# Optimization experiments

Hardware: AMD Instinct MI355X
Metric: run time of the kernel (lower is better)

The kernel has to match this reference:

```python
import jax, jax.numpy as jnp
import numpy as np

N = 100000      # total nodes in batched graph
E_RAND = 1600000  # random edges (avg degree 16); self-loops appended -> E = E_RAND + N
B = 1024        # number of graphs / descriptor batch
DIN, D2D, D3D = 128, 200, 100
DG, DH = 20, 64
H1, H2 = 128, 32
EPS = 1e-5


def _lin_init(key, fan_in, fan_out):
    k1, k2 = jax.random.split(key)
    bound = 1.0 / np.sqrt(fan_in)
    W = jax.random.uniform(k1, (fan_in, fan_out), jnp.float32, -bound, bound)
    b = jax.random.uniform(k2, (fan_out,), jnp.float32, -bound, bound)
    return W, b


def setup_inputs() -> dict:
    key = jax.random.key(0)
    ks = jax.random.split(key, 16)
    feat = jax.random.normal(ks[0], (N, DIN), jnp.float32)
    src_r = jax.random.randint(ks[1], (E_RAND,), 0, N, jnp.int32)
    dst_r = jax.random.randint(ks[2], (E_RAND,), 0, N, jnp.int32)
    loop = jnp.arange(N, dtype=jnp.int32)
    src = jnp.concatenate([src_r, loop])  # self-loops: every node has in-degree >= 1
    dst = jnp.concatenate([dst_r, loop])
    graph_id = ((jnp.arange(N, dtype=jnp.int64) * B) // N).astype(jnp.int32)  # sorted, all B nonempty
    desc_2d = jax.random.normal(ks[3], (B, D2D), jnp.float32)
    desc_3d = jax.random.normal(ks[4], (B, D3D), jnp.float32)
    Wg1, bg1 = _lin_init(ks[5], DIN, 100)
    Wg2, bg2 = _lin_init(ks[6], 100, DG)
    Wpg, bpg = _lin_init(ks[7], DG, DH)
    Wp2, bp2 = _lin_init(ks[8], D2D, DH)
    gain = np.sqrt(6.0 / (DH + DH))
    W2 = jax.random.uniform(ks[9], (DH, DH), jnp.float32, -gain, gain)  # xavier_uniform
    Wf1, bf1 = _lin_init(ks[10], 2 * DH, H1)
    Wf2, bf2 = _lin_init(ks[11], H1, H2)
    Wf3, bf3 = _lin_init(ks[12], H2, 1)
    return dict(feat=feat, src=src, dst=dst, graph_id=graph_id,
                desc_2d=desc_2d, desc_3d=desc_3d,
                Wg1=Wg1, bg1=bg1, Wg2=Wg2, bg2=bg2,
                Wpg=Wpg, bpg=bpg, Wp2=Wp2, bp2=bp2, W2=W2,
                Wf1=Wf1, bf1=bf1, Wf2=Wf2, bf2=bf2, Wf3=Wf3, bf3=bf3,
                bn1_g=jnp.ones((H1,), jnp.float32), bn1_b=jnp.zeros((H1,), jnp.float32),
                bn2_g=jnp.ones((H2,), jnp.float32), bn2_b=jnp.zeros((H2,), jnp.float32))


def _gcn(h, W, b, src, dst):
    # copy_u -> mailbox mean: segment-mean of source feats over destination
    msg = h[src]                                               # [E, d] gather
    s = jax.ops.segment_sum(msg, dst, num_segments=N)          # [N, d]
    deg = jax.ops.segment_sum(jnp.ones((src.shape[0], 1), h.dtype), dst, num_segments=N)
    accum = s / jnp.maximum(deg, 1.0)
    return jax.nn.relu(accum @ W + b)


def _bn(x, g, b):  # BatchNorm1d, training-mode batch stats (biased var)
    mu = jnp.mean(x, axis=0)
    var = jnp.mean(jnp.square(x - mu), axis=0)
    return g * (x - mu) * jax.lax.rsqrt(var + EPS) + b


def reference(feat, src, dst, graph_id, desc_2d, desc_3d,
              Wg1, bg1, Wg2, bg2, Wpg, bpg, Wp2, bp2, W2,
              Wf1, bf1, Wf2, bf2, Wf3, bf3, bn1_g, bn1_b, bn2_g, bn2_b):
    h = _gcn(feat, Wg1, bg1, src, dst)        # relu(GCN1) -> [N,100]
    h = _gcn(h, Wg2, bg2, src, dst)           # relu(GCN2) -> [N,20]
    # dgl.mean_nodes: per-graph mean
    hs = jax.ops.segment_sum(h, graph_id, num_segments=B)
    cnt = jax.ops.segment_sum(jnp.ones((N, 1), h.dtype), graph_id, num_segments=B)
    hg = hs / jnp.maximum(cnt, 1.0)           # [B, 20]
    h_g = hg @ Wpg + bpg                      # [B, 64]
    h_d = desc_2d @ Wp2 + bp2                 # [B, 64]
    gate_vec = jax.nn.sigmoid((h_g @ W2) * h_d)
    v2 = gate_vec * h_d
    fusion = jnp.concatenate([h_g, v2], axis=-1)   # [B, 128]
    out = jax.nn.relu(_bn(fusion @ Wf1 + bf1, bn1_g, bn1_b))
    out = jax.nn.relu(_bn(out @ Wf2 + bf2, bn2_g, bn2_b))
    return out @ Wf3 + bf3                    # [B, 1]
```

## Files before the change

### kernel.cpp

```cpp
#include <hip/hip_runtime.h>
#include <math.h>

#define N_NODES 100000
#define B_GRAPH 1024
#define NBKT 391
#define NBLK 416
#define CAP 6000

typedef unsigned short ushort_t;
typedef unsigned int uint_t;
typedef __attribute__((ext_vector_type(8))) short short8v;
typedef __attribute__((ext_vector_type(4))) float f32x4;

static inline size_t alignup(size_t x){ return (x + 255) & ~(size_t)255; }

__device__ inline float bf2f(ushort_t u){
  union{ uint_t i; float f; } v; v.i = ((uint_t)u) << 16; return v.f;
}
__device__ inline float bflo(uint_t u){
  union{ uint_t i; float f; } v; v.i = u << 16; return v.f;
}
__device__ inline float bfhi(uint_t u){
  union{ uint_t i; float f; } v; v.i = u & 0xffff0000u; return v.f;
}
__device__ inline ushort_t f2bf(float f){
  union{ float f; uint_t i; } v; v.f = f;
  uint_t b = v.i;
  b += 0x7fffu + ((b >> 16) & 1u);
  return (ushort_t)(b >> 16);
}
__device__ inline uint_t packbf(float a, float b){
  return (uint_t)f2bf(a) | ((uint_t)f2bf(b) << 16);
}

__global__ __launch_bounds__(256) void k_hist(const int* __restrict__ dst,
                                              int* __restrict__ hist_g, int* __restrict__ btot,
                                              int E, int CH){
  __shared__ int h[NBKT];
  int blk = blockIdx.x, t = threadIdx.x;
  for (int i = t; i < NBKT; i += 256) h[i] = 0;
  __syncthreads();
  int s = blk*CH, e = s + CH; if (e > E) e = E;
  for (int i = s + t; i < e; i += 256) atomicAdd(&h[dst[i] >> 8], 1);
  __syncthreads();
  for (int i = t; i < NBKT; i += 256){
    int v = h[i];
    hist_g[i*NBLK + blk] = v;
    if (v) atomicAdd(&btot[i], v);
  }
}

__global__ __launch_bounds__(512) void k_scanb(const int* __restrict__ btot, int* __restrict__ bbase){
  __shared__ int sc[512];
  int t = threadIdx.x;
  int v = (t < NBKT) ? btot[t] : 0;
  sc[t] = v; __syncthreads();
  for (int off = 1; off < 512; off <<= 1){
    int u = (t >= off) ? sc[t-off] : 0;
    __syncthreads();
    sc[t] += u;
    __syncthreads();
  }
  if (t < NBKT) bbase[t] = sc[t] - v;
  if (t == NBKT-1) bbase[NBKT] = sc[t];
}

__global__ __launch_bounds__(512) void k_offs(const int* __restrict__ hist_g, const int* __restrict__ bbase,
                                              int* __restrict__ offs){
  __shared__ int sc[512];
  int b = blockIdx.x, t = threadIdx.x;
  int v = (t < NBLK) ? hist_g[b*NBLK + t] : 0;
  sc[t] = v; __syncthreads();
  for (int off = 1; off < 512; off <<= 1){
    int u = (t >= off) ? sc[t-off] : 0;
    __syncthreads();
    sc[t] += u;
    __syncthreads();
  }
  if (t < NBLK) offs[b*NBLK + t] = bbase[b] + sc[t] - v;
}

__global__ __launch_bounds__(256) void k_scatter(const int* __restrict__ src, const int* __restrict__ dst,
                                                 const int* __restrict__ offs, uint2* __restrict__ pairs,
                                                 int E, int CH){
  __shared__ int base[NBKT];
  int blk = blockIdx.x, t = threadIdx.x;
  for (int i = t; i < NBKT; i += 256) base[i] = offs[i*NBLK + blk];
  __syncthreads();
  int s = blk*CH, e = s + CH; if (e > E) e = E;
  for (int i = s + t; i < e; i += 256){
    int d = dst[i];
    int pos = atomicAdd(&base[d >> 8], 1);
    uint2 p; p.x = (uint_t)src[i]; p.y = (uint_t)d;
    pairs[pos] = p;
  }
}

__global__ __launch_bounds__(256) void k_final(const uint2* __restrict__ pairs, const int* __restrict__ bbase,
                                               int* __restrict__ rp, int* __restrict__ col){
  __shared__ uint2 buf[CAP];
  __shared__ int dcnt[256];
  __shared__ int sc[256];
  __shared__ int dpos[256];
  int b = blockIdx.x, t = threadIdx.x;
  int s = bbase[b], e = bbase[b+1], n = e - s;
  dcnt[t] = 0;
  const uint2* P;
  if (n <= CAP){
    for (int i = t; i < n; i += 256) buf[i] = pairs[s + i];
    P = buf;
  } else {
    P = pairs + s;
  }
  __syncthreads();
  for (int i = t; i < n; i += 256) atomicAdd(&dcnt[P[i].y & 255], 1);
  __syncthreads();
  int v = dcnt[t];
  sc[t] = v; __syncthreads();
  for (int off = 1; off < 256; off <<= 1){
    int u = (t >= off) ? sc[t-off] : 0;
    __syncthreads();
    sc[t] += u;
    __syncthreads();
  }
  int ex = sc[t] - v;
  int node = b*256 + t;
  if (node <= N_NODES) rp[node] = s + ex;
  dpos[t] = s + ex;
  __syncthreads();
  for (int i = t; i < n; i += 256){
    uint2 pr = P[i];
    int pos = atomicAdd(&dpos[pr.y & 255], 1);
    col[pos] = (int)pr.x;
  }
}

__global__ __launch_bounds__(256) void k_cvt(const float* __restrict__ feat, ushort_t* __restrict__ fb, int n8){
  int i = blockIdx.x*256 + threadIdx.x;
  if (i >= n8) return;
  const float4* f4 = reinterpret_cast<const float4*>(feat + (size_t)i*8);
  float4 x = f4[0], y = f4[1];
  uint4 o;
  o.x = packbf(x.x, x.y); o.y = packbf(x.z, x.w);
  o.z = packbf(y.x, y.y); o.w = packbf(y.z, y.w);
  reinterpret_cast<uint4*>(fb)[i] = o;
}

__global__ __launch_bounds__(256) void k_packw(const float* __restrict__ W, ushort_t* __restrict__ wpk){
  int idx = blockIdx.x*256 + threadIdx.x;
  if (idx >= 7*4*64) return;
  int l = idx & 63;
  int s = (idx >> 6) & 3;
  int ct = idx >> 8;
  int colj = ct*16 + (l & 15);
  int kbase = 32*s + ((l >> 4) << 3);
  #pragma unroll
  for (int j = 0; j < 8; j++){
    float w = (colj < 100) ? W[(kbase + j)*100 + colj] : 0.f;
    wpk[idx*8 + j] = f2bf(w);
  }
}

__global__ __launch_bounds__(256) void k_gemm1m(const ushort_t* __restrict__ fb, const ushort_t* __restrict__ wpk,
                                                ushort_t* __restrict__ t1, int Nn){
  int wid = threadIdx.x >> 6;
  int lane = threadIdx.x & 63;
  int rt = blockIdx.x*4 + wid;
  int row0 = rt*16;
  if (row0 >= Nn) return;
  short8v a[4];
  const ushort_t* arow = fb + (size_t)(row0 + (lane & 15))*128 + ((lane >> 4) << 3);
  #pragma unroll
  for (int s = 0; s < 4; s++)
    a[s] = *reinterpret_cast<const short8v*>(arow + 32*s);
  const short8v* bfrag = reinterpret_cast<const short8v*>(wpk);
  for (int ct = 0; ct < 7; ct++){
    f32x4 acc = {0.f, 0.f, 0.f, 0.f};
    #pragma unroll
    for (int s = 0; s < 4; s++){
      short8v b = bfrag[(ct*4 + s)*64 + lane];
      acc = __builtin_amdgcn_mfma_f32_16x16x32_bf16(a[s], b, acc, 0, 0, 0);
    }
    int colj = ct*16 + (lane & 15);
    if (colj < 100){
      ushort_t* base = t1 + colj;
      #pragma unroll
      for (int r = 0; r < 4; r++){
        int row = row0 + ((lane >> 4) << 2) + r;
        base[(size_t)row*100] = f2bf(acc[r]);
      }
    }
  }
}

__global__ __launch_bounds__(256) void k_agg1(const uint_t* __restrict__ t1u, const int* __restrict__ rp,
                                              const int* __restrict__ col, const float* __restrict__ bias,
                                              uint_t* __restrict__ h1u, int Nn){
  int lane = threadIdx.x & 63;
  int node = blockIdx.x*4 + (threadIdx.x >> 6);
  if (node >= Nn) return;
  int rs = rp[node], re = rp[node+1];
  int d2 = lane < 50 ? lane : 49;
  float slo0=0.f, slo1=0.f, shi0=0.f, shi1=0.f;
  for (int base = rs; base < re; base += 64){
    int idx = base + lane;
    int colv = col[idx < re ? idx : re-1];
    int m = re - base; if (m > 64) m = 64;
    int e = 0;
    for (; e + 4 <= m; e += 4){
      int c0 = __shfl(colv, e+0), c1 = __shfl(colv, e+1);
      int c2 = __shfl(colv, e+2), c3 = __shfl(colv, e+3);
      uint_t u0 = t1u[(size_t)c0*50 + d2];
      uint_t u1 = t1u[(size_t)c1*50 + d2];
      uint_t u2 = t1u[(size_t)c2*50 + d2];
      uint_t u3 = t1u[(size_t)c3*50 + d2];
      slo0 += bflo(u0); shi0 += bfhi(u0);
      slo1 += bflo(u1); shi1 += bfhi(u1);
      slo0 += bflo(u2); shi0 += bfhi(u2);
      slo1 += bflo(u3); shi1 += bfhi(u3);
    }
    for (; e < m; e++){
      int c = __shfl(colv, e);
      uint_t u = t1u[(size_t)c*50 + d2];
      slo0 += bflo(u); shi0 += bfhi(u);
    }
  }
  if (lane < 50){
    float inv = 1.f/(float)(re - rs);
    float vlo = (slo0 + slo1)*inv + bias[2*lane];
    float vhi = (shi0 + shi1)*inv + bias[2*lane + 1];
    vlo = vlo > 0.f ? vlo : 0.f;
    vhi = vhi > 0.f ? vhi : 0.f;
    h1u[(size_t)node*50 + lane] = packbf(vlo, vhi);
  }
}

__global__ __launch_bounds__(256) void k_gemm2(const uint_t* __restrict__ h1u, const float* __restrict__ W,
                                               ushort_t* __restrict__ t2, int Nn){
  int row = blockIdx.x*256 + threadIdx.x;
  if (row >= Nn) return;
  const uint2* xb = reinterpret_cast<const uint2*>(h1u + (size_t)row*50);
  float acc[20];
  #pragma unroll
  for (int j = 0; j < 20; j++) acc[j] = 0.f;
  #pragma unroll 5
  for (int q = 0; q < 25; q++){
    uint2 u = xb[q];
    float fx = bflo(u.x), fy = bfhi(u.x), fz = bflo(u.y), fw = bfhi(u.y);
    const float* w0 = W + q*80;
    #pragma unroll
    for (int j = 0; j < 20; j++){
      float a = acc[j];
      a = fmaf(fx, w0[j],      a);
      a = fmaf(fy, w0[20 + j], a);
      a = fmaf(fz, w0[40 + j], a);
      a = fmaf(fw, w0[60 + j], a);
      acc[j] = a;
    }
  }
  uint2* o = reinterpret_cast<uint2*>(t2 + (size_t)row*20);
  #pragma unroll
  for (int j = 0; j < 5; j++){
    uint2 v; v.x = packbf(acc[4*j], acc[4*j+1]); v.y = packbf(acc[4*j+2], acc[4*j+3]);
    o[j] = v;
  }
}

__global__ __launch_bounds__(256) void k_agg2(const uint_t* __restrict__ t2u, const int* __restrict__ rp,
                                              const int* __restrict__ col, const float* __restrict__ bias,
                                              float2* __restrict__ h2, int Nn){
  int tid = threadIdx.x;
  int node = blockIdx.x*16 + (tid >> 4);
  int l16 = tid & 15;
  if (node >= Nn) return;
  int rs = rp[node], re = rp[node+1];
  int d2 = l16 < 10 ? l16 : 9;
  int grpb = (tid & 63) & ~15;
  float slo0=0.f, slo1=0.f, shi0=0.f, shi1=0.f;
  for (int base = rs; base < re; base += 16){
    int idx = base + l16;
    int colv = col[idx < re ? idx : re-1];
    int m = re - base; if (m > 16) m = 16;
    int e = 0;
    for (; e + 4 <= m; e += 4){
      int c0 = __shfl(colv, grpb+e+0), c1 = __shfl(colv, grpb+e+1);
      int c2 = __shfl(colv, grpb+e+2), c3 = __shfl(colv, grpb+e+3);
      uint_t u0 = t2u[(size_t)c0*10 + d2];
      uint_t u1 = t2u[(size_t)c1*10 + d2];
      uint_t u2 = t2u[(size_t)c2*10 + d2];
      uint_t u3 = t2u[(size_t)c3*10 + d2];
      slo0 += bflo(u0); shi0 += bfhi(u0);
      slo1 += bflo(u1); shi1 += bfhi(u1);
      slo0 += bflo(u2); shi0 += bfhi(u2);
      slo1 += bflo(u3); shi1 += bfhi(u3);
    }
    for (; e < m; e++){
      int c = __shfl(colv, grpb+e);
      uint_t u = t2u[(size_t)c*10 + d2];
      slo0 += bflo(u); shi0 += bfhi(u);
    }
  }
  if (l16 < 10){
    float inv = 1.f/(float)(re - rs);
    float vlo = (slo0 + slo1)*inv + bias[2*l16];
    float vhi = (shi0 + shi1)*inv + bias[2*l16 + 1];
    vlo = vlo > 0.f ? vlo : 0.f;
    vhi = vhi > 0.f ? vhi : 0.f;
    float2 v; v.x = vlo; v.y = vhi;
    h2[(size_t)node*10 + l16] = v;
  }
}

__global__ __launch_bounds__(256) void k_gmean(const float* __restrict__ h2, float* __restrict__ hg){
  __shared__ float red[240];
  int g = blockIdx.x;
  int t = threadIdx.x;
  int s = (int)(((long long)g      * N_NODES + B_GRAPH - 1) / B_GRAPH);
  int e = (int)(((long long)(g+1)  * N_NODES + B_GRAPH - 1) / B_GRAPH);
  if (t < 240){
    int d  = t % 20;
    int r0 = t / 20;
    float acc = 0.f;
    for (int n = s + r0; n < e; n += 12) acc += h2[(size_t)n*20 + d];
    red[t] = acc;
  }
  __syncthreads();
  if (t < 20){
    float acc = 0.f;
    #pragma unroll
    for (int r = 0; r < 12; r++) acc += red[r*20 + t];
    hg[g*20 + t] = acc / (float)(e - s);
  }
}

__global__ __launch_bounds__(256) void k_head1(const float* __restrict__ hg, const float* __restrict__ Wpg,
                                               const float* __restrict__ bpg, const float* __restrict__ desc2,
                                               const float* __restrict__ Wp2, const float* __restrict__ bp2,
                                               float* __restrict__ hG, float* __restrict__ hD){
  int idx = blockIdx.x*256 + threadIdx.x;
  if (idx >= B_GRAPH*64) return;
  int r = idx >> 6, d = idx & 63;
  float a = bpg[d];
  for (int k = 0; k < 20; k++) a = fmaf(hg[r*20 + k], Wpg[k*64 + d], a);
  hG[r*64 + d] = a;
  float c = bp2[d];
  for (int k = 0; k < 200; k++) c = fmaf(desc2[r*200 + k], Wp2[k*64 + d], c);
  hD[r*64 + d] = c;
}

__global__ __launch_bounds__(256) void k_head2(const float* __restrict__ hG, const float* __restrict__ hD,
                                               const float* __restrict__ W2, float* __restrict__ fus){
  int idx = blockIdx.x*256 + threadIdx.x;
  if (idx >= B_GRAPH*64) return;
  int r = idx >> 6, d = idx & 63;
  float x = 0.f;
  for (int k = 0; k < 64; k++) x = fmaf(hG[r*64 + k], W2[k*64 + d], x);
  float hd = hD[r*64 + d];
  float gv = 1.f / (1.f + expf(-x*hd));
  fus[r*128 + d]      = hG[r*64 + d];
  fus[r*128 + 64 + d] = gv*hd;
}

__global__ __launch_bounds__(256) void k_tr(const float* __restrict__ X, float* __restrict__ XT){
  __shared__ float tile[32][33];
  int rb = blockIdx.x >> 2;
  int cb = blockIdx.x & 3;
  int tx = threadIdx.x & 31;
  int ty = threadIdx.x >> 5;
  #pragma unroll
  for (int i = 0; i < 4; i++){
    int r = rb*32 + ty + 8*i;
    tile[ty + 8*i][tx] = X[(size_t)r*128 + cb*32 + tx];
  }
  __syncthreads();
  #pragma unroll
  for (int i = 0; i < 4; i++){
    int c = cb*32 + ty + 8*i;
    XT[(size_t)c*1024 + rb*32 + tx] = tile[tx][ty + 8*i];
  }
}

__global__ __launch_bounds__(256) void k_bnt(const float* __restrict__ XT, const float* __restrict__ W,
                                             const float* __restrict__ bias, const float* __restrict__ gam,
                                             const float* __restrict__ bet, float* __restrict__ YT,
                                             int Kin, int Jout){
  int j = blockIdx.x;
  int t = threadIdx.x;
  float b0 = bias[j];
  float4 z; z.x = b0; z.y = b0; z.z = b0; z.w = b0;
  for (int k = 0; k < Kin; k++){
    float4 x = reinterpret_cast<const float4*>(XT + (size_t)k*1024)[t];
    float wv = W[k*Jout + j];
    z.x = fmaf(x.x, wv, z.x);
    z.y = fmaf(x.y, wv, z.y);
    z.z = fmaf(x.z, wv, z.z);
    z.w = fmaf(x.w, wv, z.w);
  }
  float s = z.x+z.y+z.z+z.w;
  float q = z.x*z.x+z.y*z.y+z.z*z.z+z.w*z.w;
  __shared__ float rs_[256], rq_[256];
  rs_[t] = s; rq_[t] = q; __syncthreads();
  for (int o = 128; o > 0; o >>= 1){
    if (t < o){ rs_[t] += rs_[t+o]; rq_[t] += rq_[t+o]; }
    __syncthreads();
  }
  float mu  = rs_[0] * (1.f/1024.f);
  float var = rq_[0] * (1.f/1024.f) - mu*mu;
  float inv = 1.f / sqrtf(var + 1e-5f);
  float gj = gam[j], bj = bet[j];
  float4 y;
  y.x = gj*(z.x-mu)*inv + bj; y.x = y.x > 0.f ? y.x : 0.f;
  y.y = gj*(z.y-mu)*inv + bj; y.y = y.y > 0.f ? y.y : 0.f;
  y.z = gj*(z.z-mu)*inv + bj; y.z = y.z > 0.f ? y.z : 0.f;
  y.w = gj*(z.w-mu)*inv + bj; y.w = y.w > 0.f ? y.w : 0.f;
  reinterpret_cast<float4*>(YT + (size_t)j*1024)[t] = y;
}

__global__ __launch_bounds__(256) void k_out(const float* __restrict__ y2T, const float* __restrict__ Wf3,
                                             const float* __restrict__ bf3, float* __restrict__ out){
  int r = blockIdx.x*256 + threadIdx.x;
  if (r >= B_GRAPH) return;
  float a = bf3[0];
  #pragma unroll
  for (int k = 0; k < 32; k++) a = fmaf(y2T[k*1024 + r], Wf3[k], a);
  out[r] = a;
}

extern "C" void kernel_launch(void* const* d_in, const int* in_sizes, int n_in,
                              void* d_out, int out_size, void* d_ws, size_t ws_size,
                              hipStream_t stream){
  const float* feat  = (const float*)d_in[0];
  const int*   src   = (const int*)d_in[1];
  const int*   dst   = (const int*)d_in[2];
  const float* desc2 = (const float*)d_in[4];
  const float* Wg1   = (const float*)d_in[6];
  const float* bg1   = (const float*)d_in[7];
  const float* Wg2   = (const float*)d_in[8];
  const float* bg2   = (const float*)d_in[9];
  const float* Wpg   = (const float*)d_in[10];
  const float* bpg   = (const float*)d_in[11];
  const float* Wp2   = (const float*)d_in[12];
  const float* bp2   = (const float*)d_in[13];
  const float* W2    = (const float*)d_in[14];
  const float* Wf1   = (const float*)d_in[15];
  const float* bf1   = (const float*)d_in[16];
  const float* Wf2   = (const float*)d_in[17];
  const float* bf2   = (const float*)d_in[18];
  const float* Wf3   = (const float*)d_in[19];
  const float* bf3   = (const float*)d_in[20];
  const float* bn1g  = (const float*)d_in[21];
  const float* bn1b  = (const float*)d_in[22];
  const float* bn2g  = (const float*)d_in[23];
  const float* bn2b  = (const float*)d_in[24];
  float* out = (float*)d_out;
  const int E = in_sizes[1];

  char* w = (char*)d_ws;
  int* rp     = (int*)w; w += alignup((size_t)(N_NODES+1)*4);
  int* col    = (int*)w; w += alignup((size_t)E*4);
  int* hist_g = (int*)w; w += alignup((size_t)NBKT*NBLK*4);
  int* offs   = (int*)w; w += alignup((size_t)NBKT*NBLK*4);
  int* btot   = (int*)w; w += alignup((size_t)NBKT*4);
  int* bbase  = (int*)w; w += alignup((size_t)(NBKT+1)*4);
  ushort_t* wpk = (ushort_t*)w; w += alignup((size_t)7*4*64*8*2);
  ushort_t* t1 = (ushort_t*)w; w += alignup((size_t)N_NODES*100*2);
  char* regionA = w; w += alignup((size_t)N_NODES*128*2);
  ushort_t* t2 = (ushort_t*)w; w += alignup((size_t)N_NODES*20*2);
  float* h2   = (float*)w; w += alignup((size_t)N_NODES*20*4);
  float* hg  = (float*)w; w += alignup((size_t)B_GRAPH*20*4);
  float* hG  = (float*)w; w += alignup((size_t)B_GRAPH*64*4);
  float* hD  = (float*)w; w += alignup((size_t)B_GRAPH*64*4);
  float* fus = (float*)w; w += alignup((size_t)B_GRAPH*128*4);
  float* fusT= (float*)w; w += alignup((size_t)B_GRAPH*128*4);
  float* y1T = (float*)w; w += alignup((size_t)B_GRAPH*128*4);
  float* y2T = (float*)w; w += alignup((size_t)B_GRAPH*32*4);
  uint2* pairs   = (uint2*)regionA;
  ushort_t* fb   = (ushort_t*)regionA;
  uint_t* h1u    = (uint_t*)regionA;

  const int CH = (E + NBLK - 1)/NBLK;

  hipMemsetAsync(btot, 0, (size_t)NBKT*sizeof(int), stream);
  k_hist   <<<NBLK, 256, 0, stream>>>(dst, hist_g, btot, E, CH);
  k_scanb  <<<1,    512, 0, stream>>>(btot, bbase);
  k_offs   <<<NBKT, 512, 0, stream>>>(hist_g, bbase, offs);
  k_scatter<<<NBLK, 256, 0, stream>>>(src, dst, offs, pairs, E, CH);
  k_final  <<<NBKT, 256, 0, stream>>>(pairs, bbase, rp, col);

  k_cvt    <<<(N_NODES*128/8 + 255)/256, 256, 0, stream>>>(feat, fb, N_NODES*128/8);
  k_packw  <<<7, 256, 0, stream>>>(Wg1, wpk);
  k_gemm1m <<<(N_NODES/16 + 3)/4, 256, 0, stream>>>(fb, wpk, t1, N_NODES);
  k_agg1   <<<(N_NODES+3)/4, 256, 0, stream>>>((const uint_t*)t1, rp, col, bg1, h1u, N_NODES);
  k_gemm2  <<<(N_NODES+255)/256, 256, 0, stream>>>(h1u, Wg2, t2, N_NODES);
  k_agg2   <<<(N_NODES+15)/16, 256, 0, stream>>>((const uint_t*)t2, rp, col, bg2, (float2*)h2, N_NODES);

  k_gmean  <<<B_GRAPH, 256, 0, stream>>>(h2, hg);
  k_head1  <<<(B_GRAPH*64)/256, 256, 0, stream>>>(hg, Wpg, bpg, desc2, Wp2, bp2, hG, hD);
  k_head2  <<<(B_GRAPH*64)/256, 256, 0, stream>>>(hG, hD, W2, fus);
  k_tr     <<<128, 256, 0, stream>>>(fus, fusT);
  k_bnt    <<<128, 256, 0, stream>>>(fusT, Wf1, bf1, bn1g, bn1b, y1T, 128, 128);
  k_bnt    <<<32, 256, 0, stream>>>(y1T, Wf2, bf2, bn2g, bn2b, y2T, 128, 32);
  k_out    <<<4, 256, 0, stream>>>(y2T, Wf3, bf3, out);
}
```

Baseline: 299.9 us.

## Fuse CSR scan, bf16 convert and head kernels; pack edge pairs; widen agg1 loads

```diff
diff --git a/kernel.cpp b/kernel.cpp
--- a/kernel.cpp
+++ b/kernel.cpp
@@ -14,9 +14,6 @@
 
 static inline size_t alignup(size_t x){ return (x + 255) & ~(size_t)255; }
 
-__device__ inline float bf2f(ushort_t u){
-  union{ uint_t i; float f; } v; v.i = ((uint_t)u) << 16; return v.f;
-}
 __device__ inline float bflo(uint_t u){
   union{ uint_t i; float f; } v; v.i = u << 16; return v.f;
 }
@@ -50,25 +47,16 @@
   }
 }
 
-__global__ __launch_bounds__(512) void k_scanb(const int* __restrict__ btot, int* __restrict__ bbase){
-  __shared__ int sc[512];
-  int t = threadIdx.x;
-  int v = (t < NBKT) ? btot[t] : 0;
-  sc[t] = v; __syncthreads();
-  for (int off = 1; off < 512; off <<= 1){
-    int u = (t >= off) ? sc[t-off] : 0;
-    __syncthreads();
-    sc[t] += u;
-    __syncthreads();
-  }
-  if (t < NBKT) bbase[t] = sc[t] - v;
-  if (t == NBKT-1) bbase[NBKT] = sc[t];
-}
-
-__global__ __launch_bounds__(512) void k_offs(const int* __restrict__ hist_g, const int* __restrict__ bbase,
-                                              int* __restrict__ offs){
+__global__ __launch_bounds__(512) void k_offs(const int* __restrict__ hist_g, const int* __restrict__ btot,
+                                              int* __restrict__ offs, int* __restrict__ bbase){
   __shared__ int sc[512];
   int b = blockIdx.x, t = threadIdx.x;
+  int acc = 0;
+  for (int i = t; i < b; i += 512) acc += btot[i];
+  sc[t] = acc; __syncthreads();
+  for (int o = 256; o > 0; o >>= 1){ if (t < o) sc[t] += sc[t+o]; __syncthreads(); }
+  int bb = sc[0];
+  __syncthreads();
   int v = (t < NBLK) ? hist_g[b*NBLK + t] : 0;
   sc[t] = v; __syncthreads();
   for (int off = 1; off < 512; off <<= 1){
@@ -77,11 +65,13 @@
     sc[t] += u;
     __syncthreads();
   }
-  if (t < NBLK) offs[b*NBLK + t] = bbase[b] + sc[t] - v;
+  if (t < NBLK) offs[b*NBLK + t] = bb + sc[t] - v;
+  if (t == 0) bbase[b] = bb;
+  if (b == NBKT-1 && t == NBLK-1) bbase[NBKT] = bb + sc[t];
 }
 
 __global__ __launch_bounds__(256) void k_scatter(const int* __restrict__ src, const int* __restrict__ dst,
-                                                 const int* __restrict__ offs, uint2* __restrict__ pairs,
+                                                 const int* __restrict__ offs, uint_t* __restrict__ pairs,
                                                  int E, int CH){
   __shared__ int base[NBKT];
   int blk = blockIdx.x, t = threadIdx.x;
@@ -91,21 +81,20 @@
   for (int i = s + t; i < e; i += 256){
     int d = dst[i];
     int pos = atomicAdd(&base[d >> 8], 1);
-    uint2 p; p.x = (uint_t)src[i]; p.y = (uint_t)d;
-    pairs[pos] = p;
-  }
-}
-
-__global__ __launch_bounds__(256) void k_final(const uint2* __restrict__ pairs, const int* __restrict__ bbase,
+    pairs[pos] = (uint_t)src[i] | ((uint_t)(d & 255) << 17);
+  }
+}
+
+__global__ __launch_bounds__(256) void k_final(const uint_t* __restrict__ pairs, const int* __restrict__ bbase,
                                                int* __restrict__ rp, int* __restrict__ col){
-  __shared__ uint2 buf[CAP];
+  __shared__ uint_t buf[CAP];
   __shared__ int dcnt[256];
   __shared__ int sc[256];
   __shared__ int dpos[256];
   int b = blockIdx.x, t = threadIdx.x;
   int s = bbase[b], e = bbase[b+1], n = e - s;
   dcnt[t] = 0;
-  const uint2* P;
+  const uint_t* P;
   if (n <= CAP){
     for (int i = t; i < n; i += 256) buf[i] = pairs[s + i];
     P = buf;
@@ -113,7 +102,7 @@
     P = pairs + s;
   }
   __syncthreads();
-  for (int i = t; i < n; i += 256) atomicAdd(&dcnt[P[i].y & 255], 1);
+  for (int i = t; i < n; i += 256) atomicAdd(&dcnt[P[i] >> 17], 1);
   __syncthreads();
   int v = dcnt[t];
   sc[t] = v; __syncthreads();
@@ -129,21 +118,10 @@
   dpos[t] = s + ex;
   __syncthreads();
   for (int i = t; i < n; i += 256){
-    uint2 pr = P[i];
-    int pos = atomicAdd(&dpos[pr.y & 255], 1);
-    col[pos] = (int)pr.x;
-  }
-}
-
-__global__ __launch_bounds__(256) void k_cvt(const float* __restrict__ feat, ushort_t* __restrict__ fb, int n8){
-  int i = blockIdx.x*256 + threadIdx.x;
-  if (i >= n8) return;
-  const float4* f4 = reinterpret_cast<const float4*>(feat + (size_t)i*8);
-  float4 x = f4[0], y = f4[1];
-  uint4 o;
-  o.x = packbf(x.x, x.y); o.y = packbf(x.z, x.w);
-  o.z = packbf(y.x, y.y); o.w = packbf(y.z, y.w);
-  reinterpret_cast<uint4*>(fb)[i] = o;
+    uint_t pr = P[i];
+    int pos = atomicAdd(&dpos[pr >> 17], 1);
+    col[pos] = (int)(pr & 0x1FFFFu);
+  }
 }
 
 __global__ __launch_bounds__(256) void k_packw(const float* __restrict__ W, ushort_t* __restrict__ wpk){
@@ -161,7 +139,7 @@
   }
 }
 
-__global__ __launch_bounds__(256) void k_gemm1m(const ushort_t* __restrict__ fb, const ushort_t* __restrict__ wpk,
+__global__ __launch_bounds__(256) void k_gemm1m(const float* __restrict__ feat, const ushort_t* __restrict__ wpk,
                                                 ushort_t* __restrict__ t1, int Nn){
   int wid = threadIdx.x >> 6;
   int lane = threadIdx.x & 63;
@@ -169,10 +147,16 @@
   int row0 = rt*16;
   if (row0 >= Nn) return;
   short8v a[4];
-  const ushort_t* arow = fb + (size_t)(row0 + (lane & 15))*128 + ((lane >> 4) << 3);
-  #pragma unroll
-  for (int s = 0; s < 4; s++)
-    a[s] = *reinterpret_cast<const short8v*>(arow + 32*s);
+  const float* arow = feat + (size_t)(row0 + (lane & 15))*128 + ((lane >> 4) << 3);
+  #pragma unroll
+  for (int s = 0; s < 4; s++){
+    float4 f0 = *reinterpret_cast<const float4*>(arow + 32*s);
+    float4 f1 = *reinterpret_cast<const float4*>(arow + 32*s + 4);
+    union { short8v v; uint_t u[4]; } cv;
+    cv.u[0] = packbf(f0.x, f0.y); cv.u[1] = packbf(f0.z, f0.w);
+    cv.u[2] = packbf(f1.x, f1.y); cv.u[3] = packbf(f1.z, f1.w);
+    a[s] = cv.v;
+  }
   const short8v* bfrag = reinterpret_cast<const short8v*>(wpk);
   for (int ct = 0; ct < 7; ct++){
     f32x4 acc = {0.f, 0.f, 0.f, 0.f};
@@ -193,45 +177,57 @@
   }
 }
 
-__global__ __launch_bounds__(256) void k_agg1(const uint_t* __restrict__ t1u, const int* __restrict__ rp,
+__global__ __launch_bounds__(256) void k_agg1(const uint2* __restrict__ t1u2, const int* __restrict__ rp,
                                               const int* __restrict__ col, const float* __restrict__ bias,
-                                              uint_t* __restrict__ h1u, int Nn){
+                                              uint2* __restrict__ h1u2, int Nn){
   int lane = threadIdx.x & 63;
   int node = blockIdx.x*4 + (threadIdx.x >> 6);
   if (node >= Nn) return;
+  int h = lane >> 5;
+  int q = lane & 31; if (q > 24) q = 24;
   int rs = rp[node], re = rp[node+1];
-  int d2 = lane < 50 ? lane : 49;
-  float slo0=0.f, slo1=0.f, shi0=0.f, shi1=0.f;
+  float s0=0.f, s1=0.f, s2=0.f, s3=0.f;
   for (int base = rs; base < re; base += 64){
     int idx = base + lane;
     int colv = col[idx < re ? idx : re-1];
     int m = re - base; if (m > 64) m = 64;
-    int e = 0;
-    for (; e + 4 <= m; e += 4){
-      int c0 = __shfl(colv, e+0), c1 = __shfl(colv, e+1);
-      int c2 = __shfl(colv, e+2), c3 = __shfl(colv, e+3);
-      uint_t u0 = t1u[(size_t)c0*50 + d2];
-      uint_t u1 = t1u[(size_t)c1*50 + d2];
-      uint_t u2 = t1u[(size_t)c2*50 + d2];
-      uint_t u3 = t1u[(size_t)c3*50 + d2];
-      slo0 += bflo(u0); shi0 += bfhi(u0);
-      slo1 += bflo(u1); shi1 += bfhi(u1);
-      slo0 += bflo(u2); shi0 += bfhi(u2);
-      slo1 += bflo(u3); shi1 += bfhi(u3);
-    }
-    for (; e < m; e++){
-      int c = __shfl(colv, e);
-      uint_t u = t1u[(size_t)c*50 + d2];
-      slo0 += bflo(u); shi0 += bfhi(u);
-    }
-  }
-  if (lane < 50){
+    int np = m >> 1;
+    int i = 0;
+    for (; i + 4 <= np; i += 4){
+      int c0 = __shfl(colv, 2*(i+0)+h), c1 = __shfl(colv, 2*(i+1)+h);
+      int c2 = __shfl(colv, 2*(i+2)+h), c3 = __shfl(colv, 2*(i+3)+h);
+      uint2 u0 = t1u2[(size_t)c0*25 + q];
+      uint2 u1 = t1u2[(size_t)c1*25 + q];
+      uint2 u2 = t1u2[(size_t)c2*25 + q];
+      uint2 u3 = t1u2[(size_t)c3*25 + q];
+      s0 += bflo(u0.x); s1 += bfhi(u0.x); s2 += bflo(u0.y); s3 += bfhi(u0.y);
+      s0 += bflo(u1.x); s1 += bfhi(u1.x); s2 += bflo(u1.y); s3 += bfhi(u1.y);
+      s0 += bflo(u2.x); s1 += bfhi(u2.x); s2 += bflo(u2.y); s3 += bfhi(u2.y);
+      s0 += bflo(u3.x); s1 += bfhi(u3.x); s2 += bflo(u3.y); s3 += bfhi(u3.y);
+    }
+    for (; i < np; i++){
+      int c = __shfl(colv, 2*i + h);
+      uint2 u = t1u2[(size_t)c*25 + q];
+      s0 += bflo(u.x); s1 += bfhi(u.x); s2 += bflo(u.y); s3 += bfhi(u.y);
+    }
+    if ((m & 1) && h == 0){
+      int c = __shfl(colv, m-1);
+      uint2 u = t1u2[(size_t)c*25 + q];
+      s0 += bflo(u.x); s1 += bfhi(u.x); s2 += bflo(u.y); s3 += bfhi(u.y);
+    }
+  }
+  s0 += __shfl(s0, lane + 32);
+  s1 += __shfl(s1, lane + 32);
+  s2 += __shfl(s2, lane + 32);
+  s3 += __shfl(s3, lane + 32);
+  if (lane < 25){
     float inv = 1.f/(float)(re - rs);
-    float vlo = (slo0 + slo1)*inv + bias[2*lane];
-    float vhi = (shi0 + shi1)*inv + bias[2*lane + 1];
-    vlo = vlo > 0.f ? vlo : 0.f;
-    vhi = vhi > 0.f ? vhi : 0.f;
-    h1u[(size_t)node*50 + lane] = packbf(vlo, vhi);
+    float v0 = s0*inv + bias[4*lane];     v0 = v0 > 0.f ? v0 : 0.f;
+    float v1 = s1*inv + bias[4*lane + 1]; v1 = v1 > 0.f ? v1 : 0.f;
+    float v2 = s2*inv + bias[4*lane + 2]; v2 = v2 > 0.f ? v2 : 0.f;
+    float v3 = s3*inv + bias[4*lane + 3]; v3 = v3 > 0.f ? v3 : 0.f;
+    uint2 o; o.x = packbf(v0, v1); o.y = packbf(v2, v3);
+    h1u2[(size_t)node*25 + lane] = o;
   }
 }
 
@@ -333,31 +329,24 @@
   }
 }
 
-__global__ __launch_bounds__(256) void k_head1(const float* __restrict__ hg, const float* __restrict__ Wpg,
+__global__ __launch_bounds__(256) void k_headf(const float* __restrict__ hg, const float* __restrict__ Wpg,
                                                const float* __restrict__ bpg, const float* __restrict__ desc2,
                                                const float* __restrict__ Wp2, const float* __restrict__ bp2,
-                                               float* __restrict__ hG, float* __restrict__ hD){
+                                               const float* __restrict__ W2, float* __restrict__ fus){
+  __shared__ float hGs[4][64];
   int idx = blockIdx.x*256 + threadIdx.x;
-  if (idx >= B_GRAPH*64) return;
   int r = idx >> 6, d = idx & 63;
+  int rloc = (threadIdx.x >> 6);
   float a = bpg[d];
   for (int k = 0; k < 20; k++) a = fmaf(hg[r*20 + k], Wpg[k*64 + d], a);
-  hG[r*64 + d] = a;
-  float c = bp2[d];
-  for (int k = 0; k < 200; k++) c = fmaf(desc2[r*200 + k], Wp2[k*64 + d], c);
-  hD[r*64 + d] = c;
-}
-
-__global__ __launch_bounds__(256) void k_head2(const float* __restrict__ hG, const float* __restrict__ hD,
-                                               const float* __restrict__ W2, float* __restrict__ fus){
-  int idx = blockIdx.x*256 + threadIdx.x;
-  if (idx >= B_GRAPH*64) return;
-  int r = idx >> 6, d = idx & 63;
+  float hd = bp2[d];
+  for (int k = 0; k < 200; k++) hd = fmaf(desc2[r*200 + k], Wp2[k*64 + d], hd);
+  hGs[rloc][d] = a;
+  __syncthreads();
   float x = 0.f;
-  for (int k = 0; k < 64; k++) x = fmaf(hG[r*64 + k], W2[k*64 + d], x);
-  float hd = hD[r*64 + d];
+  for (int k = 0; k < 64; k++) x = fmaf(hGs[rloc][k], W2[k*64 + d], x);
   float gv = 1.f / (1.f + expf(-x*hd));
-  fus[r*128 + d]      = hG[r*64 + d];
+  fus[r*128 + d]      = a;
   fus[r*128 + 64 + d] = gv*hd;
 }
 
@@ -464,39 +453,33 @@
   int* bbase  = (int*)w; w += alignup((size_t)(NBKT+1)*4);
   ushort_t* wpk = (ushort_t*)w; w += alignup((size_t)7*4*64*8*2);
   ushort_t* t1 = (ushort_t*)w; w += alignup((size_t)N_NODES*100*2);
-  char* regionA = w; w += alignup((size_t)N_NODES*128*2);
+  char* regionA = w; w += alignup((size_t)N_NODES*50*4);
   ushort_t* t2 = (ushort_t*)w; w += alignup((size_t)N_NODES*20*2);
   float* h2   = (float*)w; w += alignup((size_t)N_NODES*20*4);
   float* hg  = (float*)w; w += alignup((size_t)B_GRAPH*20*4);
-  float* hG  = (float*)w; w += alignup((size_t)B_GRAPH*64*4);
-  float* hD  = (float*)w; w += alignup((size_t)B_GRAPH*64*4);
   float* fus = (float*)w; w += alignup((size_t)B_GRAPH*128*4);
   float* fusT= (float*)w; w += alignup((size_t)B_GRAPH*128*4);
   float* y1T = (float*)w; w += alignup((size_t)B_GRAPH*128*4);
   float* y2T = (float*)w; w += alignup((size_t)B_GRAPH*32*4);
-  uint2* pairs   = (uint2*)regionA;
-  ushort_t* fb   = (ushort_t*)regionA;
-  uint_t* h1u    = (uint_t*)regionA;
+  uint_t* pairs = (uint_t*)regionA;
+  uint_t* h1u   = (uint_t*)regionA;
 
   const int CH = (E + NBLK - 1)/NBLK;
 
   hipMemsetAsync(btot, 0, (size_t)NBKT*sizeof(int), stream);
   k_hist   <<<NBLK, 256, 0, stream>>>(dst, hist_g, btot, E, CH);
-  k_scanb  <<<1,    512, 0, stream>>>(btot, bbase);
-  k_offs   <<<NBKT, 512, 0, stream>>>(hist_g, bbase, offs);
+  k_offs   <<<NBKT, 512, 0, stream>>>(hist_g, btot, offs, bbase);
   k_scatter<<<NBLK, 256, 0, stream>>>(src, dst, offs, pairs, E, CH);
   k_final  <<<NBKT, 256, 0, stream>>>(pairs, bbase, rp, col);
 
-  k_cvt    <<<(N_NODES*128/8 + 255)/256, 256, 0, stream>>>(feat, fb, N_NODES*128/8);
   k_packw  <<<7, 256, 0, stream>>>(Wg1, wpk);
-  k_gemm1m <<<(N_NODES/16 + 3)/4, 256, 0, stream>>>(fb, wpk, t1, N_NODES);
-  k_agg1   <<<(N_NODES+3)/4, 256, 0, stream>>>((const uint_t*)t1, rp, col, bg1, h1u, N_NODES);
+  k_gemm1m <<<(N_NODES/16 + 3)/4, 256, 0, stream>>>(feat, wpk, t1, N_NODES);
+  k_agg1   <<<(N_NODES+3)/4, 256, 0, stream>>>((const uint2*)t1, rp, col, bg1, (uint2*)h1u, N_NODES);
   k_gemm2  <<<(N_NODES+255)/256, 256, 0, stream>>>(h1u, Wg2, t2, N_NODES);
   k_agg2   <<<(N_NODES+15)/16, 256, 0, stream>>>((const uint_t*)t2, rp, col, bg2, (float2*)h2, N_NODES);
 
   k_gmean  <<<B_GRAPH, 256, 0, stream>>>(h2, hg);
-  k_head1  <<<(B_GRAPH*64)/256, 256, 0, stream>>>(hg, Wpg, bpg, desc2, Wp2, bp2, hG, hD);
-  k_head2  <<<(B_GRAPH*64)/256, 256, 0, stream>>>(hG, hD, W2, fus);
+  k_headf  <<<(B_GRAPH*64)/256, 256, 0, stream>>>(hg, Wpg, bpg, desc2, Wp2, bp2, W2, fus);
   k_tr     <<<128, 256, 0, stream>>>(fus, fusT);
   k_bnt    <<<128, 256, 0, stream>>>(fusT, Wf1, bf1, bn1g, bn1b, y1T, 128, 128);
   k_bnt    <<<32, 256, 0, stream>>>(y1T, Wf2, bf2, bn2g, bn2b, y2T, 128, 32);
```

Measured after the change: 283.1 us. 5.6% less time.
